# Performance work log

Measured on AMD Instinct MI355X. Metric: run time of the kernel, lower is better.

## Reference

```python
import jax, jax.numpy as jnp
import numpy as np

BN_EPS = 1e-5


def setup_inputs() -> dict:
    key = jax.random.key(0)
    ks = jax.random.split(key, 4)
    N, V, C = 64, 512, 512
    K, OUT = 2, 512
    x = jax.random.normal(ks[0], (N, V, C), dtype=jnp.float32)
    A = jax.random.uniform(ks[1], (N, K, V, V), dtype=jnp.float32) / V
    conv_w = jax.random.normal(ks[2], (2 * OUT, C), dtype=jnp.float32) / np.sqrt(C)
    conv_b = jax.random.normal(ks[3], (2 * OUT,), dtype=jnp.float32) * 0.01
    gamma = jnp.ones((2 * OUT,), dtype=jnp.float32)
    beta = jnp.zeros((2 * OUT,), dtype=jnp.float32)
    eps_p = jnp.zeros((1,), dtype=jnp.float32)
    return {"x": x, "A": A, "conv_w": conv_w, "conv_b": conv_b,
            "gamma": gamma, "beta": beta, "eps_p": eps_p}


def reference(x, A, conv_w, conv_b, gamma, beta, eps_p):
    # x: (N, V, C); A: (N, K, V, V)
    N, V, C = x.shape
    K = A.shape[1]
    # 1x1 Conv1d over nodes: (N, 2*out, V)
    h = jnp.einsum('nvc,oc->nov', x, conv_w) + conv_b[None, :, None]
    # BatchNorm1d, training-mode batch stats (biased variance, per channel)
    mean = jnp.mean(h, axis=(0, 2), keepdims=True)
    var = jnp.var(h, axis=(0, 2), keepdims=True)
    h = (h - mean) * jax.lax.rsqrt(var + BN_EPS) * gamma[None, :, None] + beta[None, :, None]
    c2 = h.shape[1]
    h = h.reshape(N, K, c2 // K, V)  # (N, K, out, V)
    # graph propagation: x A then (x A) A^T, contracted over node dims
    t = jnp.einsum('nkcm,nkme->nkce', h, A)
    At = jnp.transpose(A, (0, 1, 3, 2))
    y = jnp.einsum('nkce,nkem->ncm', t, At)  # (N, out, V)
    out = (1.0 + eps_p[0]) * x + jnp.transpose(y, (0, 2, 1))
    return out, At
```

## Files before the change

kernel.cpp:

```cpp
#include <hip/hip_runtime.h>
#include <stdint.h>

typedef __bf16 bf16x8 __attribute__((ext_vector_type(8)));
typedef float f32x4 __attribute__((ext_vector_type(4)));
typedef unsigned short us4_t __attribute__((ext_vector_type(4)));
typedef unsigned short us8_t __attribute__((ext_vector_type(8)));

#define LDSK 40

__device__ __forceinline__ unsigned short f2bf(float f) {
  __bf16 b = (__bf16)f;
  return __builtin_bit_cast(unsigned short, b);
}
__device__ __forceinline__ float bf2f(unsigned short u) {
  union { uint32_t u; float f; } v; v.u = ((uint32_t)u) << 16;
  return v.f;
}

__device__ __forceinline__ void gload16(const void* g, void* l) {
  __builtin_amdgcn_global_load_lds(
      (const __attribute__((address_space(1))) void*)g,
      (__attribute__((address_space(3))) void*)l, 16, 0, 0);
}

__device__ __forceinline__ void stage_tile(const unsigned short* g, size_t ldg,
                                           unsigned short* lds, int wid, int lane) {
#pragma unroll
  for (int i = 0; i < 2; ++i) {
    int seg = wid * 2 + i;
    const unsigned short* gp = g + (size_t)(seg * 16 + (lane >> 2)) * ldg + (lane & 3) * 8;
    gload16(gp, lds + seg * 512);
  }
}

__device__ __forceinline__ void mfma_step(const unsigned short* As, const unsigned short* Bs,
                                          int ldb, f32x4 (*acc)[4],
                                          int wr, int wc, int lr, int lk) {
  bf16x8 a[4], b[4];
#pragma unroll
  for (int mi = 0; mi < 4; ++mi)
    a[mi] = *(const bf16x8*)(As + (wr + mi * 16 + lr) * 32 + lk * 8);
#pragma unroll
  for (int ni = 0; ni < 4; ++ni)
    b[ni] = *(const bf16x8*)(Bs + (wc + ni * 16 + lr) * ldb + lk * 8);
#pragma unroll
  for (int mi = 0; mi < 4; ++mi)
#pragma unroll
    for (int ni = 0; ni < 4; ++ni)
      acc[mi][ni] = __builtin_amdgcn_mfma_f32_16x16x32_bf16(a[mi], b[ni], acc[mi][ni], 0, 0, 0);
}

__device__ __forceinline__ void bn_block(
    const unsigned short* __restrict__ H, const float* __restrict__ gamma,
    const float* __restrict__ beta, float* __restrict__ sc_sh,
    int o, int tid, float* r1, float* r2) {
  const int g = tid >> 6, l = tid & 63;
  float s1 = 0.f, s2 = 0.f;
  for (int step = 0; step < 16; ++step) {
    int n = g + step * 4;
    const us8_t* row = (const us8_t*)(H + ((size_t)n * 1024 + o) * 512);
    us8_t v = row[l];
#pragma unroll
    for (int j = 0; j < 8; ++j) { float f = bf2f(v[j]); s1 += f; s2 += f * f; }
  }
  r1[tid] = s1; r2[tid] = s2;
  __syncthreads();
  for (int off = 128; off > 0; off >>= 1) {
    if (tid < off) { r1[tid] += r1[tid + off]; r2[tid] += r2[tid + off]; }
    __syncthreads();
  }
  if (tid == 0) {
    float mean = r1[0] * (1.0f / 32768.0f);
    float var = r2[0] * (1.0f / 32768.0f) - mean * mean;
    float s = gamma[o] * rsqrtf(var + 1e-5f);
    sc_sh[o] = s;
    sc_sh[1024 + o] = beta[o] - mean * s;
  }
}

__global__ __launch_bounds__(256) void k_convert(
    const float* __restrict__ X, const float* __restrict__ W,
    unsigned short* __restrict__ Xb, unsigned short* __restrict__ Wb) {
  const size_t idx = (size_t)blockIdx.x * 256 + threadIdx.x;
  const size_t stride = (size_t)gridDim.x * 256;
  for (size_t i = idx; i < (size_t)16777216 / 8; i += stride) {
    float4 f0 = ((const float4*)X)[2 * i], f1 = ((const float4*)X)[2 * i + 1];
    us8_t w = { f2bf(f0.x), f2bf(f0.y), f2bf(f0.z), f2bf(f0.w),
                f2bf(f1.x), f2bf(f1.y), f2bf(f1.z), f2bf(f1.w) };
    ((us8_t*)Xb)[i] = w;
  }
  for (size_t i = idx; i < (size_t)524288 / 8; i += stride) {
    float4 f0 = ((const float4*)W)[2 * i], f1 = ((const float4*)W)[2 * i + 1];
    us8_t w = { f2bf(f0.x), f2bf(f0.y), f2bf(f0.z), f2bf(f0.w),
                f2bf(f1.x), f2bf(f1.y), f2bf(f1.z), f2bf(f1.w) };
    ((us8_t*)Wb)[i] = w;
  }
}

__global__ __launch_bounds__(256) void k_gemm1(
    const unsigned short* __restrict__ Wb, const unsigned short* __restrict__ Xb,
    const float* __restrict__ convb, unsigned short* __restrict__ H) {
  __shared__ unsigned short As[4096];
  __shared__ unsigned short Bs[4096];
  const int tid = threadIdx.x;
  const int L = blockIdx.x;
  const int xcd = L & 7, slot = L >> 3;
  const int n = xcd * 8 + (slot >> 5);
  const int tile = slot & 31;
  const int tm = tile >> 2, tn = tile & 3;
  const unsigned short* gA = Wb + (size_t)tm * 128 * 512;
  const unsigned short* gB = Xb + ((size_t)n * 512 + tn * 128) * 512;
  const int lane = tid & 63, wid = tid >> 6;
  const int wr = (wid >> 1) * 64, wc = (wid & 1) * 64;
  const int lr = lane & 15, lk = lane >> 4;
  f32x4 acc[4][4] = {};
  for (int k0 = 0; k0 < 512; k0 += 32) {
    stage_tile(gA + k0, 512, As, wid, lane);
    stage_tile(gB + k0, 512, Bs, wid, lane);
    __syncthreads();
    mfma_step(As, Bs, 32, acc, wr, wc, lr, lk);
    __syncthreads();
  }
  unsigned short* Hn = H + (size_t)n * 1024 * 512;
#pragma unroll
  for (int mi = 0; mi < 4; ++mi)
#pragma unroll
    for (int i = 0; i < 4; ++i) {
      int o = tm * 128 + wr + mi * 16 + lk * 4 + i;
      float bias = convb[o];
#pragma unroll
      for (int ni = 0; ni < 4; ++ni) {
        int v = tn * 128 + wc + ni * 16 + lr;
        Hn[(size_t)o * 512 + v] = f2bf(acc[mi][ni][i] + bias);
      }
    }
}

__global__ __launch_bounds__(256) void k_bn_at_ab(
    const unsigned short* __restrict__ H, const float* __restrict__ gamma,
    const float* __restrict__ beta, float* __restrict__ sc_sh,
    const float* __restrict__ A, float* __restrict__ At,
    unsigned short* __restrict__ Ab) {
  const int tid = threadIdx.x;
  if (blockIdx.x < 1024) {
    __shared__ float r1[256], r2[256];
    bn_block(H, gamma, beta, sc_sh, blockIdx.x, tid, r1, r2);
  } else {
    __shared__ float tile[64][65];
    const int tIdx = blockIdx.x - 1024;
    const int nk = tIdx >> 6;
    const int e0 = (tIdx & 7) * 64, m0 = ((tIdx >> 3) & 7) * 64;
    const float* src = A + (size_t)nk * 262144;
    float* dst = At + (size_t)nk * 262144;
    unsigned short* ab = Ab + (size_t)nk * 262144;
#pragma unroll
    for (int j = 0; j < 4; ++j) {
      int ch = tid + j * 256;
      int r = ch >> 4, c4 = (ch & 15) * 4;
      float4 f = *(const float4*)(src + (size_t)(m0 + r) * 512 + e0 + c4);
      tile[r][c4] = f.x; tile[r][c4 + 1] = f.y; tile[r][c4 + 2] = f.z; tile[r][c4 + 3] = f.w;
      us4_t u = { f2bf(f.x), f2bf(f.y), f2bf(f.z), f2bf(f.w) };
      *(us4_t*)(ab + (size_t)(m0 + r) * 512 + e0 + c4) = u;
    }
    __syncthreads();
#pragma unroll
    for (int j = 0; j < 4; ++j) {
      int ch = tid + j * 256;
      int e = ch >> 4, m4 = (ch & 15) * 4;
      float4 g = { tile[m4][e], tile[m4 + 1][e], tile[m4 + 2][e], tile[m4 + 3][e] };
      *(float4*)(dst + (size_t)(e0 + e) * 512 + m0 + m4) = g;
    }
  }
}

__global__ __launch_bounds__(256) void k_bn_convA(
    const unsigned short* __restrict__ H, const float* __restrict__ gamma,
    const float* __restrict__ beta, float* __restrict__ sc_sh,
    const float* __restrict__ A, unsigned short* __restrict__ Ab) {
  const int tid = threadIdx.x;
  if (blockIdx.x < 1024) {
    __shared__ float r1[256], r2[256];
    bn_block(H, gamma, beta, sc_sh, blockIdx.x, tid, r1, r2);
  } else {
    const size_t idx = (size_t)(blockIdx.x - 1024) * 256 + tid;
    const size_t stride = (size_t)2048 * 256;
    for (size_t i = idx; i < (size_t)33554432 / 8; i += stride) {
      float4 f0 = ((const float4*)A)[2 * i], f1 = ((const float4*)A)[2 * i + 1];
      us8_t w = { f2bf(f0.x), f2bf(f0.y), f2bf(f0.z), f2bf(f0.w),
                  f2bf(f1.x), f2bf(f1.y), f2bf(f1.z), f2bf(f1.w) };
      ((us8_t*)Ab)[i] = w;
    }
  }
}

__global__ __launch_bounds__(256) void k_bn(
    const unsigned short* __restrict__ H, const float* __restrict__ gamma,
    const float* __restrict__ beta, float* __restrict__ sc_sh) {
  __shared__ float r1[256], r2[256];
  bn_block(H, gamma, beta, sc_sh, blockIdx.x, threadIdx.x, r1, r2);
}

__global__ __launch_bounds__(256) void k_convertA(
    const float* __restrict__ A, unsigned short* __restrict__ Ab) {
  const size_t idx = (size_t)blockIdx.x * 256 + threadIdx.x;
  const size_t stride = (size_t)gridDim.x * 256;
  for (size_t i = idx; i < (size_t)33554432 / 8; i += stride) {
    float4 f0 = ((const float4*)A)[2 * i], f1 = ((const float4*)A)[2 * i + 1];
    us8_t w = { f2bf(f0.x), f2bf(f0.y), f2bf(f0.z), f2bf(f0.w),
                f2bf(f1.x), f2bf(f1.y), f2bf(f1.z), f2bf(f1.w) };
    ((us8_t*)Ab)[i] = w;
  }
}

__global__ __launch_bounds__(256) void k_affine(
    unsigned short* __restrict__ H, const float* __restrict__ sc_sh) {
  const size_t idx = (size_t)blockIdx.x * 256 + threadIdx.x;
  const size_t stride = (size_t)gridDim.x * 256;
  const size_t total8 = (size_t)64 * 1024 * 512 / 8;
  for (size_t i = idx; i < total8; i += stride) {
    size_t base = i * 8;
    int o = (int)((base >> 9) & 1023);
    float sc = sc_sh[o], sh = sc_sh[1024 + o];
    us8_t v = ((const us8_t*)H)[i];
    us8_t w;
#pragma unroll
    for (int j = 0; j < 8; ++j) w[j] = f2bf(fmaf(bf2f(v[j]), sc, sh));
    ((us8_t*)H)[i] = w;
  }
}

__global__ __launch_bounds__(256) void k_aat(
    const unsigned short* __restrict__ Ab, unsigned short* __restrict__ B2) {
  __shared__ unsigned short As[4096];
  __shared__ unsigned short Bs[4096];
  const int tid = threadIdx.x;
  const int L = blockIdx.x;
  const int xcd = L & 7, slot = L >> 3;
  const int nk = xcd * 16 + (slot >> 4);
  const int tile = slot & 15;
  const int tm = tile >> 2, tn = tile & 3;
  const unsigned short* Ank = Ab + (size_t)nk * 262144;
  const unsigned short* gA = Ank + (size_t)tm * 128 * 512;
  const unsigned short* gB = Ank + (size_t)tn * 128 * 512;
  const int lane = tid & 63, wid = tid >> 6;
  const int wr = (wid >> 1) * 64, wc = (wid & 1) * 64;
  const int lr = lane & 15, lk = lane >> 4;
  f32x4 acc[4][4] = {};
  for (int k0 = 0; k0 < 512; k0 += 32) {
    stage_tile(gA + k0, 512, As, wid, lane);
    stage_tile(gB + k0, 512, Bs, wid, lane);
    __syncthreads();
    mfma_step(As, Bs, 32, acc, wr, wc, lr, lk);
    __syncthreads();
  }
  unsigned short* Bn = B2 + (size_t)nk * 262144;
#pragma unroll
  for (int mi = 0; mi < 4; ++mi)
#pragma unroll
    for (int i = 0; i < 4; ++i) {
      int m = tm * 128 + wr + mi * 16 + lk * 4 + i;
#pragma unroll
      for (int ni = 0; ni < 4; ++ni) {
        int mp = tn * 128 + wc + ni * 16 + lr;
        Bn[(size_t)m * 512 + mp] = f2bf(acc[mi][ni][i]);
      }
    }
}

template <bool AFFINE>
__global__ __launch_bounds__(256) void k_gemm3(
    const unsigned short* __restrict__ B2, const unsigned short* __restrict__ H,
    const float* __restrict__ sc_sh, const float* __restrict__ X,
    const float* __restrict__ epsp, float* __restrict__ out) {
  __shared__ unsigned short As[4096];
  __shared__ unsigned short Bs[64 * LDSK];
  __shared__ float s_sc[2][64], s_sh[2][64];
  const int tid = threadIdx.x;
  const int L = blockIdx.x;
  const int xcd = L & 7, slot = L >> 3;
  const int n = xcd * 8 + (slot >> 5);
  const int tile = slot & 31;
  const int tm = tile >> 3, tn = tile & 7;
  const int lane = tid & 63, wid = tid >> 6;
  const int wr = (wid >> 1) * 64, wc = (wid & 1) * 32;
  const int lr = lane & 15, lk = lane >> 4;
  if (AFFINE) {
    if (tid < 128) {
      int kkq = tid >> 6, r = tid & 63;
      s_sc[kkq][r] = sc_sh[kkq * 512 + tn * 64 + r];
      s_sh[kkq][r] = sc_sh[1024 + kkq * 512 + tn * 64 + r];
    }
    __syncthreads();
  }
  f32x4 acc[4][2] = {};
  for (int kk = 0; kk < 2; ++kk) {
    const unsigned short* gA = B2 + ((size_t)(n * 2 + kk) * 512 + tm * 128) * 512;
    const unsigned short* gB = H + ((size_t)n * 1024 + kk * 512 + tn * 64) * 512;
    for (int k0 = 0; k0 < 512; k0 += 32) {
      stage_tile(gA + k0, 512, As, wid, lane);
      {
        int r = tid >> 2, c8 = (tid & 3) * 8;
        us8_t v = *(const us8_t*)(gB + (size_t)r * 512 + k0 + c8);
        if (AFFINE) {
          float sc = s_sc[kk][r], sh = s_sh[kk][r];
          us8_t w;
#pragma unroll
          for (int j = 0; j < 8; ++j) w[j] = f2bf(fmaf(bf2f(v[j]), sc, sh));
          *(us8_t*)&Bs[r * LDSK + c8] = w;
        } else {
          *(us8_t*)&Bs[r * LDSK + c8] = v;
        }
      }
      __syncthreads();
      bf16x8 a[4], b[2];
#pragma unroll
      for (int mi = 0; mi < 4; ++mi)
        a[mi] = *(const bf16x8*)(As + (wr + mi * 16 + lr) * 32 + lk * 8);
#pragma unroll
      for (int ni = 0; ni < 2; ++ni)
        b[ni] = *(const bf16x8*)(Bs + (wc + ni * 16 + lr) * LDSK + lk * 8);
#pragma unroll
      for (int mi = 0; mi < 4; ++mi)
#pragma unroll
        for (int ni = 0; ni < 2; ++ni)
          acc[mi][ni] = __builtin_amdgcn_mfma_f32_16x16x32_bf16(a[mi], b[ni], acc[mi][ni], 0, 0, 0);
      __syncthreads();
    }
  }
  const float e1 = 1.0f + epsp[0];
#pragma unroll
  for (int mi = 0; mi < 4; ++mi)
#pragma unroll
    for (int i = 0; i < 4; ++i) {
      int v = tm * 128 + wr + mi * 16 + lk * 4 + i;
#pragma unroll
      for (int ni = 0; ni < 2; ++ni) {
        int c = tn * 64 + wc + ni * 16 + lr;
        size_t idx = ((size_t)n * 512 + v) * 512 + c;
        out[idx] = fmaf(e1, X[idx], acc[mi][ni][i]);
      }
    }
}

__global__ __launch_bounds__(256) void k_at(
    const float* __restrict__ A, float* __restrict__ At) {
  __shared__ float tile[64][65];
  const int nk = blockIdx.z;
  const int e0 = blockIdx.x * 64, m0 = blockIdx.y * 64;
  const float* src = A + (size_t)nk * 262144;
  float* dst = At + (size_t)nk * 262144;
  const int t = threadIdx.x;
#pragma unroll
  for (int j = 0; j < 4; ++j) {
    int ch = t + j * 256;
    int r = ch >> 4, c4 = (ch & 15) * 4;
    float4 f = *(const float4*)(src + (size_t)(m0 + r) * 512 + e0 + c4);
    tile[r][c4] = f.x; tile[r][c4 + 1] = f.y; tile[r][c4 + 2] = f.z; tile[r][c4 + 3] = f.w;
  }
  __syncthreads();
#pragma unroll
  for (int j = 0; j < 4; ++j) {
    int ch = t + j * 256;
    int e = ch >> 4, m4 = (ch & 15) * 4;
    float4 g = { tile[m4][e], tile[m4 + 1][e], tile[m4 + 2][e], tile[m4 + 3][e] };
    *(float4*)(dst + (size_t)(e0 + e) * 512 + m0 + m4) = g;
  }
}

extern "C" void kernel_launch(void* const* d_in, const int* in_sizes, int n_in,
                              void* d_out, int out_size, void* d_ws, size_t ws_size,
                              hipStream_t stream) {
  const float* x      = (const float*)d_in[0];
  const float* A      = (const float*)d_in[1];
  const float* conv_w = (const float*)d_in[2];
  const float* conv_b = (const float*)d_in[3];
  const float* gamma  = (const float*)d_in[4];
  const float* beta   = (const float*)d_in[5];
  const float* eps_p  = (const float*)d_in[6];

  float* out = (float*)d_out;
  float* At  = out + (size_t)16777216;

  unsigned short* Xb = (unsigned short*)out;
  unsigned short* Wb = Xb + (size_t)16777216;
  unsigned short* AbO = (unsigned short*)out;

  const size_t WS_BIG = (size_t)2 * 67108864 + 8192;
  if (ws_size >= WS_BIG) {
    unsigned short* H  = (unsigned short*)d_ws;
    unsigned short* B2 = H + (size_t)33554432;
    float* sc_sh = (float*)(B2 + (size_t)33554432);
    k_convert    <<<2048, 256, 0, stream>>>(x, conv_w, Xb, Wb);
    k_gemm1      <<<2048, 256, 0, stream>>>(Wb, Xb, conv_b, H);
    k_bn_at_ab   <<<9216, 256, 0, stream>>>(H, gamma, beta, sc_sh, A, At, AbO);
    k_aat        <<<2048, 256, 0, stream>>>(AbO, B2);
    k_gemm3<true><<<2048, 256, 0, stream>>>(B2, H, sc_sh, x, eps_p, out);
    return;
  }

  unsigned short* B2 = (unsigned short*)At;
  unsigned short* H  = (unsigned short*)(At + (size_t)16777216);
  float* wsf = (float*)d_ws;

  if (ws_size >= 8192) {
    float* sc_sh = wsf;
    k_convert    <<<2048, 256, 0, stream>>>(x, conv_w, Xb, Wb);
    k_gemm1      <<<2048, 256, 0, stream>>>(Wb, Xb, conv_b, H);
    k_bn_convA   <<<3072, 256, 0, stream>>>(H, gamma, beta, sc_sh, A, AbO);
    k_aat        <<<2048, 256, 0, stream>>>(AbO, B2);
    k_gemm3<true><<<2048, 256, 0, stream>>>(B2, H, sc_sh, x, eps_p, out);
  } else {
    float* sc_sh = out;
    k_convert     <<<2048, 256, 0, stream>>>(x, conv_w, Xb, Wb);
    k_gemm1       <<<2048, 256, 0, stream>>>(Wb, Xb, conv_b, H);
    k_bn          <<<1024, 256, 0, stream>>>(H, gamma, beta, sc_sh);
    k_affine      <<<2048, 256, 0, stream>>>(H, sc_sh);
    k_convertA    <<<2048, 256, 0, stream>>>(A, AbO);
    k_aat         <<<2048, 256, 0, stream>>>(AbO, B2);
    k_gemm3<false><<<2048, 256, 0, stream>>>(B2, H, nullptr, x, eps_p, out);
  }
  k_at<<<dim3(8, 8, 128), 256, 0, stream>>>(A, At);
}
```

Before: 295.0 us.

## Move BN affine into extra blocks of A·Aᵀ kernel and widen gemm3 tiles

The BatchNorm scale/shift on H is no longer applied in the final GEMM's operand load. Extra blocks appended to the A·Aᵀ GEMM launch now apply it in place, running alongside the GEMM blocks. The final GEMM then uses 512-thread blocks with 128x128 tiles, and both operands are staged with direct global-to-LDS loads, removing the per-element register conversion and padded LDS layout. The cost is an extra read-modify-write pass over H, and LDS bank conflicts become possible with the unpadded B layout.

```diff
diff --git a/kernel.cpp b/kernel.cpp
--- a/kernel.cpp
+++ b/kernel.cpp
@@ -5,8 +5,6 @@
 typedef float f32x4 __attribute__((ext_vector_type(4)));
 typedef unsigned short us4_t __attribute__((ext_vector_type(4)));
 typedef unsigned short us8_t __attribute__((ext_vector_type(8)));
-
-#define LDSK 40
 
 __device__ __forceinline__ unsigned short f2bf(float f) {
   __bf16 b = (__bf16)f;
@@ -267,49 +265,86 @@
     }
 }
 
-template <bool AFFINE>
-__global__ __launch_bounds__(256) void k_gemm3(
-    const unsigned short* __restrict__ B2, const unsigned short* __restrict__ H,
-    const float* __restrict__ sc_sh, const float* __restrict__ X,
-    const float* __restrict__ epsp, float* __restrict__ out) {
+__global__ __launch_bounds__(256) void k_aat_affine(
+    const unsigned short* __restrict__ Ab, unsigned short* __restrict__ B2,
+    unsigned short* __restrict__ H, const float* __restrict__ sc_sh) {
+  const int tid = threadIdx.x;
+  if (blockIdx.x >= 2048) {
+    const size_t idx = (size_t)(blockIdx.x - 2048) * 256 + tid;
+    const size_t stride = (size_t)2048 * 256;
+    const size_t total8 = (size_t)64 * 1024 * 512 / 8;
+    for (size_t i = idx; i < total8; i += stride) {
+      size_t base = i * 8;
+      int o = (int)((base >> 9) & 1023);
+      float sc = sc_sh[o], sh = sc_sh[1024 + o];
+      us8_t v = ((const us8_t*)H)[i];
+      us8_t w;
+#pragma unroll
+      for (int j = 0; j < 8; ++j) w[j] = f2bf(fmaf(bf2f(v[j]), sc, sh));
+      ((us8_t*)H)[i] = w;
+    }
+    return;
+  }
   __shared__ unsigned short As[4096];
-  __shared__ unsigned short Bs[64 * LDSK];
-  __shared__ float s_sc[2][64], s_sh[2][64];
-  const int tid = threadIdx.x;
+  __shared__ unsigned short Bs[4096];
   const int L = blockIdx.x;
   const int xcd = L & 7, slot = L >> 3;
-  const int n = xcd * 8 + (slot >> 5);
-  const int tile = slot & 31;
-  const int tm = tile >> 3, tn = tile & 7;
+  const int nk = xcd * 16 + (slot >> 4);
+  const int tile = slot & 15;
+  const int tm = tile >> 2, tn = tile & 3;
+  const unsigned short* Ank = Ab + (size_t)nk * 262144;
+  const unsigned short* gA = Ank + (size_t)tm * 128 * 512;
+  const unsigned short* gB = Ank + (size_t)tn * 128 * 512;
   const int lane = tid & 63, wid = tid >> 6;
-  const int wr = (wid >> 1) * 64, wc = (wid & 1) * 32;
+  const int wr = (wid >> 1) * 64, wc = (wid & 1) * 64;
   const int lr = lane & 15, lk = lane >> 4;
-  if (AFFINE) {
-    if (tid < 128) {
-      int kkq = tid >> 6, r = tid & 63;
-      s_sc[kkq][r] = sc_sh[kkq * 512 + tn * 64 + r];
-      s_sh[kkq][r] = sc_sh[1024 + kkq * 512 + tn * 64 + r];
-    }
-    __syncthreads();
-  }
+  f32x4 acc[4][4] = {};
+  for (int k0 = 0; k0 < 512; k0 += 32) {
+    stage_tile(gA + k0, 512, As, wid, lane);
+    stage_tile(gB + k0, 512, Bs, wid, lane);
+    __syncthreads();
+    mfma_step(As, Bs, 32, acc, wr, wc, lr, lk);
+    __syncthreads();
+  }
+  unsigned short* Bn = B2 + (size_t)nk * 262144;
+#pragma unroll
+  for (int mi = 0; mi < 4; ++mi)
+#pragma unroll
+    for (int i = 0; i < 4; ++i) {
+      int m = tm * 128 + wr + mi * 16 + lk * 4 + i;
+#pragma unroll
+      for (int ni = 0; ni < 4; ++ni) {
+        int mp = tn * 128 + wc + ni * 16 + lr;
+        Bn[(size_t)m * 512 + mp] = f2bf(acc[mi][ni][i]);
+      }
+    }
+}
+
+__global__ __launch_bounds__(512) void k_gemm3(
+    const unsigned short* __restrict__ B2, const unsigned short* __restrict__ H,
+    const float* __restrict__ X, const float* __restrict__ epsp,
+    float* __restrict__ out) {
+  __shared__ unsigned short As[4096];
+  __shared__ unsigned short Bs[4096];
+  const int tid = threadIdx.x;
+  const int L = blockIdx.x;
+  const int xcd = L & 7, slot = L >> 3;
+  const int n = xcd * 8 + (slot >> 4);
+  const int tile = slot & 15;
+  const int tm = tile >> 2, tn = tile & 3;
+  const int lane = tid & 63, wid = tid >> 6;
+  const int wr = (wid >> 2) * 64, wc = (wid & 3) * 32;
+  const int lr = lane & 15, lk = lane >> 4;
   f32x4 acc[4][2] = {};
   for (int kk = 0; kk < 2; ++kk) {
     const unsigned short* gA = B2 + ((size_t)(n * 2 + kk) * 512 + tm * 128) * 512;
-    const unsigned short* gB = H + ((size_t)n * 1024 + kk * 512 + tn * 64) * 512;
+    const unsigned short* gB = H + ((size_t)n * 1024 + kk * 512 + tn * 128) * 512;
     for (int k0 = 0; k0 < 512; k0 += 32) {
-      stage_tile(gA + k0, 512, As, wid, lane);
       {
-        int r = tid >> 2, c8 = (tid & 3) * 8;
-        us8_t v = *(const us8_t*)(gB + (size_t)r * 512 + k0 + c8);
-        if (AFFINE) {
-          float sc = s_sc[kk][r], sh = s_sh[kk][r];
-          us8_t w;
-#pragma unroll
-          for (int j = 0; j < 8; ++j) w[j] = f2bf(fmaf(bf2f(v[j]), sc, sh));
-          *(us8_t*)&Bs[r * LDSK + c8] = w;
-        } else {
-          *(us8_t*)&Bs[r * LDSK + c8] = v;
-        }
+        int r = wid * 16 + (lane >> 2);
+        int c = (lane & 3) * 8;
+        gload16(gA + (size_t)r * 512 + k0 + c, As + wid * 512);
+        gload16(gB + (size_t)r * 512 + k0 + c, Bs + wid * 512);
       }
       __syncthreads();
       bf16x8 a[4], b[2];
@@ -318,7 +353,7 @@
         a[mi] = *(const bf16x8*)(As + (wr + mi * 16 + lr) * 32 + lk * 8);
 #pragma unroll
       for (int ni = 0; ni < 2; ++ni)
-        b[ni] = *(const bf16x8*)(Bs + (wc + ni * 16 + lr) * LDSK + lk * 8);
+        b[ni] = *(const bf16x8*)(Bs + (wc + ni * 16 + lr) * 32 + lk * 8);
 #pragma unroll
       for (int mi = 0; mi < 4; ++mi)
 #pragma unroll
@@ -335,7 +370,7 @@
       int v = tm * 128 + wr + mi * 16 + lk * 4 + i;
 #pragma unroll
       for (int ni = 0; ni < 2; ++ni) {
-        int c = tn * 64 + wc + ni * 16 + lr;
+        int c = tn * 128 + wc + ni * 16 + lr;
         size_t idx = ((size_t)n * 512 + v) * 512 + c;
         out[idx] = fmaf(e1, X[idx], acc[mi][ni][i]);
       }
@@ -390,11 +425,11 @@
     unsigned short* H  = (unsigned short*)d_ws;
     unsigned short* B2 = H + (size_t)33554432;
     float* sc_sh = (float*)(B2 + (size_t)33554432);
-    k_convert    <<<2048, 256, 0, stream>>>(x, conv_w, Xb, Wb);
-    k_gemm1      <<<2048, 256, 0, stream>>>(Wb, Xb, conv_b, H);
-    k_bn_at_ab   <<<9216, 256, 0, stream>>>(H, gamma, beta, sc_sh, A, At, AbO);
-    k_aat        <<<2048, 256, 0, stream>>>(AbO, B2);
-    k_gemm3<true><<<2048, 256, 0, stream>>>(B2, H, sc_sh, x, eps_p, out);
+    k_convert     <<<2048, 256, 0, stream>>>(x, conv_w, Xb, Wb);
+    k_gemm1       <<<2048, 256, 0, stream>>>(Wb, Xb, conv_b, H);
+    k_bn_at_ab    <<<9216, 256, 0, stream>>>(H, gamma, beta, sc_sh, A, At, AbO);
+    k_aat_affine  <<<4096, 256, 0, stream>>>(AbO, B2, H, sc_sh);
+    k_gemm3       <<<1024, 512, 0, stream>>>(B2, H, x, eps_p, out);
     return;
   }
 
@@ -404,11 +439,11 @@
 
   if (ws_size >= 8192) {
     float* sc_sh = wsf;
-    k_convert    <<<2048, 256, 0, stream>>>(x, conv_w, Xb, Wb);
-    k_gemm1      <<<2048, 256, 0, stream>>>(Wb, Xb, conv_b, H);
-    k_bn_convA   <<<3072, 256, 0, stream>>>(H, gamma, beta, sc_sh, A, AbO);
-    k_aat        <<<2048, 256, 0, stream>>>(AbO, B2);
-    k_gemm3<true><<<2048, 256, 0, stream>>>(B2, H, sc_sh, x, eps_p, out);
+    k_convert     <<<2048, 256, 0, stream>>>(x, conv_w, Xb, Wb);
+    k_gemm1       <<<2048, 256, 0, stream>>>(Wb, Xb, conv_b, H);
+    k_bn_convA    <<<3072, 256, 0, stream>>>(H, gamma, beta, sc_sh, A, AbO);
+    k_aat_affine  <<<4096, 256, 0, stream>>>(AbO, B2, H, sc_sh);
+    k_gemm3       <<<1024, 512, 0, stream>>>(B2, H, x, eps_p, out);
   } else {
     float* sc_sh = out;
     k_convert     <<<2048, 256, 0, stream>>>(x, conv_w, Xb, Wb);
@@ -417,7 +452,7 @@
     k_affine      <<<2048, 256, 0, stream>>>(H, sc_sh);
     k_convertA    <<<2048, 256, 0, stream>>>(A, AbO);
     k_aat         <<<2048, 256, 0, stream>>>(AbO, B2);
-    k_gemm3<false><<<2048, 256, 0, stream>>>(B2, H, nullptr, x, eps_p, out);
+    k_gemm3       <<<1024, 512, 0, stream>>>(B2, H, x, eps_p, out);
   }
   k_at<<<dim3(8, 8, 128), 256, 0, stream>>>(A, At);
 }
```

After: 280.6 us. 1.05x faster.
